# Kernel tuning notes

Hardware: AMD Instinct MI355X
Metric: run time of the kernel (lower is better)

The kernel has to match this reference:

```python
import jax, jax.numpy as jnp
import numpy as np

B, T, C = 2, 2048, 2048
NUM_HEADS, NUM_KV_HEADS, HEAD_DIM = 16, 4, 128
ROPE_THETA = 10000.0
SOFTCAP = 50.0


def sine_table(features, length, min_timescale=1.0, max_timescale=10000.0):
    fraction = jnp.arange(0, features, 2, dtype=jnp.float32) / features
    timescale = min_timescale * (max_timescale / min_timescale) ** fraction
    sinusoid = jnp.arange(length, dtype=jnp.float32)[:, None] / timescale[None, :]
    sinusoid = jnp.concatenate([sinusoid, sinusoid], axis=-1)
    return jnp.sin(sinusoid), jnp.cos(sinusoid)


def rotate_half(x):
    x1, x2 = jnp.split(x, 2, axis=-1)
    return jnp.concatenate([-x2, x1], axis=-1)


def setup_inputs() -> dict:
    key = jax.random.key(0)
    k1, k2, k3, k4, k5 = jax.random.split(key, 5)
    x = jax.random.normal(k1, (B, T, C), dtype=jnp.float32)
    mask = jnp.tril(jnp.ones((T, T), dtype=bool))[None, None]  # causal [1,1,T,T]
    mask = jnp.broadcast_to(mask, (B, 1, T, T))
    std = 0.02
    q_kernel = std * jax.random.normal(k2, (C, NUM_HEADS * HEAD_DIM), dtype=jnp.float32)
    k_kernel = std * jax.random.normal(k3, (C, NUM_KV_HEADS * HEAD_DIM), dtype=jnp.float32)
    v_kernel = std * jax.random.normal(k4, (C, NUM_KV_HEADS * HEAD_DIM), dtype=jnp.float32)
    out_kernel = std * jax.random.normal(k5, (NUM_HEADS * HEAD_DIM, C), dtype=jnp.float32)
    return {"x": x, "mask": mask, "q_kernel": q_kernel, "k_kernel": k_kernel,
            "v_kernel": v_kernel, "out_kernel": out_kernel}


def reference(x, mask, q_kernel, k_kernel, v_kernel, out_kernel):
    _, t, c = x.shape
    r = NUM_HEADS // NUM_KV_HEADS  # GQA group size
    qp = q_kernel.reshape(c, r, NUM_KV_HEADS, HEAD_DIM)
    kp = k_kernel.reshape(c, NUM_KV_HEADS, HEAD_DIM)
    vp = v_kernel.reshape(c, NUM_KV_HEADS, HEAD_DIM)
    op = out_kernel.reshape(r, NUM_KV_HEADS, HEAD_DIM, c)
    q = jnp.einsum('bsm,mrhk->brhsk', x, qp)   # [B,r,h,T,hd]
    k = jnp.einsum('bdm,mhk->bhdk', x, kp)     # [B,h,T,hd]
    v = jnp.einsum('bdm,mhv->bhdv', x, vp)     # [B,h,T,hd]
    sin, cos = sine_table(HEAD_DIM, t, max_timescale=ROPE_THETA)  # [T,hd]
    q = q * cos + rotate_half(q) * sin  # broadcast over leading dims (time at -2)
    k = k * cos + rotate_half(k) * sin
    scale = jax.lax.rsqrt(jnp.array(HEAD_DIM, dtype=x.dtype))
    qk = jnp.einsum('brhsk,bhdk->brhsd', q, k) * scale  # [B,r,h,T,T]
    qk = jnp.tanh(qk / SOFTCAP) * SOFTCAP  # logit softcap
    m = jnp.expand_dims(mask, axis=1)  # [B,1,1,T,T]
    qk = jax.nn.softmax(qk.astype(jnp.float32), where=m).astype(x.dtype)
    qkv = jnp.einsum('brhsd,bhdv->brhsv', qk, v)
    out = jnp.einsum('brhsv,rhvm->bsm', qkv, op)
    return out
```

## Files before the change

kernel.cpp:

```cpp
#include <hip/hip_runtime.h>
#include <hip/hip_bf16.h>

typedef __hip_bfloat16 bf16;
typedef __attribute__((ext_vector_type(8))) short bf16x8;
typedef __attribute__((ext_vector_type(4))) short bf16x4;
typedef __attribute__((ext_vector_type(4))) float f32x4;

#define BATCH 2
#define SEQ 2048
#define CDIM 2048
#define NH 16
#define NKV 4
#define HD 128
#define NQKV 3072

__device__ __forceinline__ float tof(float x)  { return x; }
__device__ __forceinline__ float tof(bf16 x)   { return __bfloat162float(x); }
__device__ __forceinline__ void  stf(float* p, float v) { *p = v; }
__device__ __forceinline__ void  stf(bf16* p,  float v) { *p = __float2bfloat16(v); }

__device__ __forceinline__ void gl_lds16(const bf16* g, bf16* l) {
    typedef const __attribute__((address_space(1))) unsigned int* gp_t;
    typedef __attribute__((address_space(3))) unsigned int* lp_t;
    __builtin_amdgcn_global_load_lds((gp_t)g, (lp_t)l, 16, 0, 0);
}

__device__ __forceinline__ f32x4 mfma16x16x16_bf16(bf16x4 a, bf16x4 b, f32x4 c) {
#if __has_builtin(__builtin_amdgcn_mfma_f32_16x16x16bf16_1k)
    return __builtin_amdgcn_mfma_f32_16x16x16bf16_1k(a, b, c, 0, 0, 0);
#else
    asm volatile("v_mfma_f32_16x16x16_bf16 %0, %1, %2, %0"
                 : "+v"(c) : "v"(a), "v"(b));
    return c;
#endif
}

__device__ __forceinline__ float fast_exp2(float x) {
#if __has_builtin(__builtin_amdgcn_exp2f)
    return __builtin_amdgcn_exp2f(x);
#else
    return exp2f(x);
#endif
}

__device__ __forceinline__ float softcap_exp(float u) {
    float t2 = u * u;
    float w = fmaf(t2, -1.328448e-7f, 0.12753101f);
    return fast_exp2(u * w);
}

__global__ __launch_bounds__(256) void f2b_kernel(const float* __restrict__ in,
                                                  bf16* __restrict__ out, int n4)
{
    int i = blockIdx.x * 256 + threadIdx.x;
    if (i >= n4) return;
    float4 v = *(const float4*)&in[(size_t)i * 4];
    bf16 o[4] = {__float2bfloat16(v.x), __float2bfloat16(v.y),
                 __float2bfloat16(v.z), __float2bfloat16(v.w)};
    *(ushort4*)&out[(size_t)i * 4] = *(ushort4*)o;
}

__global__ __launch_bounds__(256) void transpose_f2b_kernel(
    const float* __restrict__ in, bf16* __restrict__ out, int R, int Cn)
{
    __shared__ float tile[64][65];
    const int r0 = blockIdx.y * 64, c0 = blockIdx.x * 64;
    for (int f = threadIdx.x; f < 4096; f += 256) {
        int r = f >> 6, c = f & 63;
        tile[r][c] = in[(size_t)(r0 + r) * Cn + c0 + c];
    }
    __syncthreads();
    for (int f = threadIdx.x; f < 4096; f += 256) {
        int r = f >> 6, c = f & 63;
        out[(size_t)(c0 + r) * R + r0 + c] = __float2bfloat16(tile[c][r]);
    }
}

__global__ __launch_bounds__(256) void vtrans_kernel(
    const bf16* __restrict__ in, bf16* __restrict__ out)
{
    __shared__ bf16 tile[64][65];
    const int b = blockIdx.z;
    const int t0 = blockIdx.y * 64, c0 = blockIdx.x * 64;
    for (int f = threadIdx.x; f < 4096; f += 256) {
        int r = f >> 6, c = f & 63;
        tile[r][c] = in[(size_t)(b * SEQ + t0 + r) * (NKV * HD) + c0 + c];
    }
    __syncthreads();
    for (int f = threadIdx.x; f < 4096; f += 256) {
        int r = f >> 6, c = f & 63;
        out[(size_t)(b * NKV * HD + c0 + r) * SEQ + t0 + c] = tile[c][r];
    }
}

__global__ __launch_bounds__(256) void gemm_qkv_kernel(
    const bf16* __restrict__ A, const bf16* __restrict__ Bt,
    bf16* __restrict__ Qr, bf16* __restrict__ Kr, bf16* __restrict__ Vr,
    int M, int K)
{
    __shared__ __align__(16) bf16 As[128 * 32];
    __shared__ __align__(16) bf16 Bs[128 * 32];

    const int tid = threadIdx.x;
    const int lane = tid & 63;
    const int wave = tid >> 6;
    const int m0 = blockIdx.y * 128;
    const int n0 = blockIdx.x * 128;
    const int wm = (wave >> 1) * 64;
    const int wn = (wave & 1) * 64;
    const int quad = lane >> 4;
    const int l16 = lane & 15;

    const int srow = tid >> 2;
    const int scol = (tid & 3) * 8;
    const bf16* Ag0 = A  + (size_t)(m0 + srow) * K + scol;
    const bf16* Ag1 = A  + (size_t)(m0 + srow + 64) * K + scol;
    const bf16* Bg0 = Bt + (size_t)(n0 + srow) * K + scol;
    const bf16* Bg1 = Bt + (size_t)(n0 + srow + 64) * K + scol;

    f32x4 acc[4][4];
#pragma unroll
    for (int mi = 0; mi < 4; ++mi)
#pragma unroll
        for (int ni = 0; ni < 4; ++ni)
            acc[mi][ni] = (f32x4){0.f, 0.f, 0.f, 0.f};

    for (int kt = 0; kt < K; kt += 32) {
        __syncthreads();
        gl_lds16(Ag0 + kt, &As[tid * 8]);
        gl_lds16(Ag1 + kt, &As[2048 + tid * 8]);
        gl_lds16(Bg0 + kt, &Bs[tid * 8]);
        gl_lds16(Bg1 + kt, &Bs[2048 + tid * 8]);
        __syncthreads();

        bf16x8 a[4], b[4];
#pragma unroll
        for (int mi = 0; mi < 4; ++mi)
            a[mi] = *(const bf16x8*)&As[(wm + mi * 16 + l16) * 32 + quad * 8];
#pragma unroll
        for (int ni = 0; ni < 4; ++ni)
            b[ni] = *(const bf16x8*)&Bs[(wn + ni * 16 + l16) * 32 + quad * 8];
#pragma unroll
        for (int mi = 0; mi < 4; ++mi)
#pragma unroll
            for (int ni = 0; ni < 4; ++ni)
                acc[mi][ni] = __builtin_amdgcn_mfma_f32_16x16x32_bf16(
                    a[mi], b[ni], acc[mi][ni], 0, 0, 0);
    }

    bf16* Cp; int Nst, cbase;
    if (n0 < 2048)      { Cp = Qr; Nst = 2048; cbase = n0; }
    else if (n0 < 2560) { Cp = Kr; Nst = 512;  cbase = n0 - 2048; }
    else                { Cp = Vr; Nst = 512;  cbase = n0 - 2560; }

#pragma unroll
    for (int mi = 0; mi < 4; ++mi)
#pragma unroll
        for (int ni = 0; ni < 4; ++ni) {
            int col = cbase + wn + ni * 16 + l16;
#pragma unroll
            for (int r = 0; r < 4; ++r) {
                int row = m0 + wm + mi * 16 + quad * 4 + r;
                Cp[(size_t)row * Nst + col] = __float2bfloat16(acc[mi][ni][r]);
            }
        }
}

template <typename TC>
__global__ __launch_bounds__(256) void gemm_mfma_bt(
    const bf16* __restrict__ A, const bf16* __restrict__ Bt, TC* __restrict__ C,
    int M, int N, int K)
{
    __shared__ __align__(16) bf16 As[128 * 32];
    __shared__ __align__(16) bf16 Bs[128 * 32];

    const int tid = threadIdx.x;
    const int lane = tid & 63;
    const int wave = tid >> 6;
    const int m0 = blockIdx.y * 128;
    const int n0 = blockIdx.x * 128;
    const int wm = (wave >> 1) * 64;
    const int wn = (wave & 1) * 64;
    const int quad = lane >> 4;
    const int l16 = lane & 15;

    const int srow = tid >> 2;
    const int scol = (tid & 3) * 8;
    const bf16* Ag0 = A  + (size_t)(m0 + srow) * K + scol;
    const bf16* Ag1 = A  + (size_t)(m0 + srow + 64) * K + scol;
    const bf16* Bg0 = Bt + (size_t)(n0 + srow) * K + scol;
    const bf16* Bg1 = Bt + (size_t)(n0 + srow + 64) * K + scol;

    f32x4 acc[4][4];
#pragma unroll
    for (int mi = 0; mi < 4; ++mi)
#pragma unroll
        for (int ni = 0; ni < 4; ++ni)
            acc[mi][ni] = (f32x4){0.f, 0.f, 0.f, 0.f};

    for (int kt = 0; kt < K; kt += 32) {
        __syncthreads();
        gl_lds16(Ag0 + kt, &As[tid * 8]);
        gl_lds16(Ag1 + kt, &As[2048 + tid * 8]);
        gl_lds16(Bg0 + kt, &Bs[tid * 8]);
        gl_lds16(Bg1 + kt, &Bs[2048 + tid * 8]);
        __syncthreads();

        bf16x8 a[4], b[4];
#pragma unroll
        for (int mi = 0; mi < 4; ++mi)
            a[mi] = *(const bf16x8*)&As[(wm + mi * 16 + l16) * 32 + quad * 8];
#pragma unroll
        for (int ni = 0; ni < 4; ++ni)
            b[ni] = *(const bf16x8*)&Bs[(wn + ni * 16 + l16) * 32 + quad * 8];
#pragma unroll
        for (int mi = 0; mi < 4; ++mi)
#pragma unroll
            for (int ni = 0; ni < 4; ++ni)
                acc[mi][ni] = __builtin_amdgcn_mfma_f32_16x16x32_bf16(
                    a[mi], b[ni], acc[mi][ni], 0, 0, 0);
    }

#pragma unroll
    for (int mi = 0; mi < 4; ++mi)
#pragma unroll
        for (int ni = 0; ni < 4; ++ni) {
            int col = n0 + wn + ni * 16 + l16;
#pragma unroll
            for (int r = 0; r < 4; ++r) {
                int row = m0 + wm + mi * 16 + quad * 4 + r;
                stf(&C[(size_t)row * N + col], acc[mi][ni][r]);
            }
        }
}

__global__ __launch_bounds__(256) void rope_kernel(bf16* __restrict__ data,
                                                   int ncols, int total_pairs)
{
    int idx = blockIdx.x * 256 + threadIdx.x;
    if (idx >= total_pairs) return;
    int half = ncols >> 1;
    int row = idx / half;
    int p = idx - row * half;
    int head = p >> 6;
    int i = p & 63;
    int t = row & (SEQ - 1);
    float inv_ts = expf(-(float)i * 0.14391156831212787f);
    float angle = (float)t * inv_ts;
    float s, c;
    sincosf(angle, &s, &c);
    size_t base = (size_t)row * ncols + head * 128 + i;
    float x1 = __bfloat162float(data[base]);
    float x2 = __bfloat162float(data[base + 64]);
    data[base]      = __float2bfloat16(x1 * c - x2 * s);
    data[base + 64] = __float2bfloat16(x2 * c + x1 * s);
}

template <bool WA>
__device__ __forceinline__ void attn_tile_compute(
    const bf16* __restrict__ Ksr, const bf16* __restrict__ Vtsr,
    const bf16x8 (&qfA)[4], const bf16x8 (&qfB)[4],
    f32x4 (&OA)[8], f32x4 (&OB)[8], float& lsumA, float& lsumB,
    int quad, int l16, int ks, bool diagA, bool diagB, int qselA, int qselB)
{
    f32x4 sA[2], sB[2];
    bf16x4 pfA[2], pfB[2];
#pragma unroll
    for (int mt = 0; mt < 2; ++mt) {
        sB[mt] = (f32x4){0.f, 0.f, 0.f, 0.f};
        if constexpr (WA) sA[mt] = (f32x4){0.f, 0.f, 0.f, 0.f};
        const int krow = (ks * 32 + mt * 16 + l16) * 128;
#pragma unroll
        for (int kk = 0; kk < 4; ++kk) {
            bf16x8 kf = *(const bf16x8*)&Ksr[krow + (((kk * 4 + quad) ^ l16) * 8)];
            sB[mt] = __builtin_amdgcn_mfma_f32_16x16x32_bf16(
                kf, qfB[kk], sB[mt], 0, 0, 0);
            if constexpr (WA)
                sA[mt] = __builtin_amdgcn_mfma_f32_16x16x32_bf16(
                    kf, qfA[kk], sA[mt], 0, 0, 0);
        }
    }
#pragma unroll
    for (int mt = 0; mt < 2; ++mt) {
        bf16 pb[4];
#pragma unroll
        for (int r = 0; r < 4; ++r) {
            float p = softcap_exp(sB[mt][r]);
            if (diagB) {
                int kl = ks * 32 + mt * 16 + quad * 4 + r;
                p = (kl <= qselB) ? p : 0.f;
            }
            lsumB += p;
            pb[r] = __float2bfloat16(p);
        }
        pfB[mt] = *(bf16x4*)pb;
        if constexpr (WA) {
            bf16 pa[4];
#pragma unroll
            for (int r = 0; r < 4; ++r) {
                float p = softcap_exp(sA[mt][r]);
                if (diagA) {
                    int kl = ks * 32 + mt * 16 + quad * 4 + r;
                    p = (kl <= qselA) ? p : 0.f;
                }
                lsumA += p;
                pa[r] = __float2bfloat16(p);
            }
            pfA[mt] = *(bf16x4*)pa;
        }
    }
#pragma unroll
    for (int dj = 0; dj < 8; ++dj) {
        const int vrow = (dj * 16 + l16) * 64;
        const int dl7 = l16 & 7;
#pragma unroll
        for (int mt = 0; mt < 2; ++mt) {
            int c16 = ks * 4 + mt * 2 + (quad >> 1);
            bf16x4 vf = *(const bf16x4*)&Vtsr[vrow + ((c16 ^ dl7) << 3)
                                              + (quad & 1) * 4];
            OB[dj] = mfma16x16x16_bf16(vf, pfB[mt], OB[dj]);
            if constexpr (WA)
                OA[dj] = mfma16x16x16_bf16(vf, pfA[mt], OA[dj]);
        }
    }
}

__global__ __launch_bounds__(512, 2) void attn_mfma10_kernel(
    const bf16* __restrict__ Q, const bf16* __restrict__ K,
    const bf16* __restrict__ Vt, bf16* __restrict__ Att)
{
    __shared__ __align__(16) char smem[70144];

    const int tid = threadIdx.x;
    const int lane = tid & 63;
    const int w = tid >> 6;
    const int ks = w >> 2;
    const int hs = (w >> 1) & 1;
    const int qw = w & 1;
    const int quad = lane >> 4;
    const int l16 = lane & 15;
    const int bh = blockIdx.y;
    const int b   = bh >> 3;
    const int kvh = (bh >> 1) & 3;
    const int pr  = bh & 1;
    const int hq  = kvh + 4 * (pr * 2 + hs);
    const int qlo = blockIdx.x;
    const int qhi = 63 - qlo;
    const int ntlo = (qlo >> 1) + 1;
    const int nthi = (qhi >> 1) + 1;
    const int q0A = qlo * 32 + qw * 16;
    const int q0B = qhi * 32 + qw * 16;

    bf16x8 qfA[4], qfB[4];
    {
        size_t ra = (size_t)(b * SEQ + q0A + l16) * (NH * HD) + hq * HD;
        size_t rb = (size_t)(b * SEQ + q0B + l16) * (NH * HD) + hq * HD;
#pragma unroll
        for (int kk = 0; kk < 4; ++kk) {
            qfA[kk] = *(const bf16x8*)&Q[ra + kk * 32 + quad * 8];
            qfB[kk] = *(const bf16x8*)&Q[rb + kk * 32 + quad * 8];
        }
    }

    f32x4 OA[8], OB[8];
#pragma unroll
    for (int dj = 0; dj < 8; ++dj) {
        OA[dj] = (f32x4){0.f, 0.f, 0.f, 0.f};
        OB[dj] = (f32x4){0.f, 0.f, 0.f, 0.f};
    }
    float lsumA = 0.f, lsumB = 0.f;

    const int qselA = (qlo & 1) * 32 + qw * 16 + l16;
    const int qselB = (qhi & 1) * 32 + qw * 16 + l16;

    const int keyK = tid >> 4;
    const int chK  = (tid & 15) ^ (keyK & 15);
    const int dV   = tid >> 3;
    const int chV  = (tid & 7) ^ (dV & 7);
    const bf16* gK = K  + (size_t)(b * SEQ + keyK) * (NKV * HD) + kvh * HD + chK * 8;
    const bf16* gV = Vt + (size_t)((b * NKV + kvh) * HD + dV) * SEQ + chV * 8;

    {
        bf16* KsW  = (bf16*)smem;
        bf16* VtsW = (bf16*)(smem + 32768);
        gl_lds16(gK,                 KsW + tid * 8);
        gl_lds16(gK + 32 * NKV * HD, KsW + 4096 + tid * 8);
        gl_lds16(gV,                 VtsW + tid * 8);
        gl_lds16(gV + 64 * SEQ,      VtsW + 4096 + tid * 8);
    }
    __syncthreads();

    int cur = 0;
    for (int jt = 0; jt < nthi; ++jt) {
        if (jt + 1 < nthi) {
            gK += 64 * NKV * HD;
            gV += 64;
            bf16* KsW  = (bf16*)(smem + (cur ^ 1) * 16384);
            bf16* VtsW = (bf16*)(smem + 32768 + (cur ^ 1) * 16384);
            gl_lds16(gK,                 KsW + tid * 8);
            gl_lds16(gK + 32 * NKV * HD, KsW + 4096 + tid * 8);
            gl_lds16(gV,                 VtsW + tid * 8);
            gl_lds16(gV + 64 * SEQ,      VtsW + 4096 + tid * 8);
        }
        const bf16* Ksr  = (const bf16*)(smem + cur * 16384);
        const bf16* Vtsr = (const bf16*)(smem + 32768 + cur * 16384);
        const bool diagA = (jt == ntlo - 1);
        const bool diagB = (jt == nthi - 1);
        if (jt < ntlo)
            attn_tile_compute<true>(Ksr, Vtsr, qfA, qfB, OA, OB, lsumA, lsumB,
                                    quad, l16, ks, diagA, diagB, qselA, qselB);
        else
            attn_tile_compute<false>(Ksr, Vtsr, qfA, qfB, OA, OB, lsumA, lsumB,
                                     quad, l16, ks, diagA, diagB, qselA, qselB);
        __syncthreads();
        cur ^= 1;
    }

    float* Osh = (float*)smem;
    float* Lsh = (float*)(smem + 69632);
    const int p = hs * 2 + qw;
    const int ob = (p * 64 + lane) * 68;
    if (ks == 1) {
#pragma unroll
        for (int dj = 0; dj < 8; ++dj) {
            *(f32x4*)&Osh[ob + dj * 4]      = OA[dj];
            *(f32x4*)&Osh[ob + 32 + dj * 4] = OB[dj];
        }
        float vA = lsumA;
        vA += __shfl_xor(vA, 16);
        vA += __shfl_xor(vA, 32);
        float vB = lsumB;
        vB += __shfl_xor(vB, 16);
        vB += __shfl_xor(vB, 32);
        if (quad == 0) {
            Lsh[p * 32 + l16]      = vA;
            Lsh[p * 32 + 16 + l16] = vB;
        }
    }
    __syncthreads();
    if (ks == 0) {
        const int b2 = bh >> 3;
        {
            float v = lsumA;
            v += __shfl_xor(v, 16);
            v += __shfl_xor(v, 32);
            v += Lsh[p * 32 + l16];
            float inv = 1.f / v;
            size_t obase = (size_t)(b2 * SEQ + q0A + l16) * (NH * HD) + hq * HD;
#pragma unroll
            for (int dj = 0; dj < 8; ++dj) {
                f32x4 o = OA[dj] + *(const f32x4*)&Osh[ob + dj * 4];
                bf16 obuf[4];
#pragma unroll
                for (int r = 0; r < 4; ++r)
                    obuf[r] = __float2bfloat16(o[r] * inv);
                *(ushort4*)&Att[obase + dj * 16 + quad * 4] = *(ushort4*)obuf;
            }
        }
        {
            float v = lsumB;
            v += __shfl_xor(v, 16);
            v += __shfl_xor(v, 32);
            v += Lsh[p * 32 + 16 + l16];
            float inv = 1.f / v;
            size_t obase = (size_t)(b2 * SEQ + q0B + l16) * (NH * HD) + hq * HD;
#pragma unroll
            for (int dj = 0; dj < 8; ++dj) {
                f32x4 o = OB[dj] + *(const f32x4*)&Osh[ob + 32 + dj * 4];
                bf16 obuf[4];
#pragma unroll
                for (int r = 0; r < 4; ++r)
                    obuf[r] = __float2bfloat16(o[r] * inv);
                *(ushort4*)&Att[obase + dj * 16 + quad * 4] = *(ushort4*)obuf;
            }
        }
    }
}

extern "C" void kernel_launch(void* const* d_in, const int* in_sizes, int n_in,
                              void* d_out, int out_size, void* d_ws, size_t ws_size,
                              hipStream_t stream) {
    const float* x        = (const float*)d_in[0];
    const float* q_kernel = (const float*)d_in[2];
    const float* k_kernel = (const float*)d_in[3];
    const float* v_kernel = (const float*)d_in[4];
    const float* o_kernel = (const float*)d_in[5];
    float* out = (float*)d_out;

    const int M = BATCH * SEQ;
    char* ws = (char*)d_ws;
    bf16* xb   = (bf16*)ws;
    bf16* Att  = xb;
    bf16* wT   = (bf16*)(ws + 16777216);
    bf16* wTq  = wT;
    bf16* wTk  = wT + (size_t)2048 * 2048;
    bf16* wTv  = wT + (size_t)2560 * 2048;
    bf16* woT  = wT;
    bf16* Vt_g = (bf16*)(ws + 25165824);
    bf16* Qr   = (bf16*)(ws + 29360128);
    bf16* Kr   = (bf16*)(ws + 46137344);
    bf16* Vr   = (bf16*)(ws + 50331648);

    f2b_kernel<<<(M * CDIM / 4 + 255) / 256, 256, 0, stream>>>(x, xb, M * CDIM / 4);
    transpose_f2b_kernel<<<dim3((NH * HD) / 64, CDIM / 64), 256, 0, stream>>>(
        q_kernel, wTq, CDIM, NH * HD);
    transpose_f2b_kernel<<<dim3((NKV * HD) / 64, CDIM / 64), 256, 0, stream>>>(
        k_kernel, wTk, CDIM, NKV * HD);
    transpose_f2b_kernel<<<dim3((NKV * HD) / 64, CDIM / 64), 256, 0, stream>>>(
        v_kernel, wTv, CDIM, NKV * HD);

    gemm_qkv_kernel<<<dim3(NQKV / 128, M / 128), 256, 0, stream>>>(
        xb, wT, Qr, Kr, Vr, M, CDIM);

    transpose_f2b_kernel<<<dim3(CDIM / 64, CDIM / 64), 256, 0, stream>>>(
        o_kernel, woT, CDIM, CDIM);

    {
        int pairs_q = M * (NH * HD / 2);
        rope_kernel<<<pairs_q / 256, 256, 0, stream>>>(Qr, NH * HD, pairs_q);
        int pairs_k = M * (NKV * HD / 2);
        rope_kernel<<<pairs_k / 256, 256, 0, stream>>>(Kr, NKV * HD, pairs_k);
    }

    vtrans_kernel<<<dim3((NKV * HD) / 64, SEQ / 64, BATCH), 256, 0, stream>>>(Vr, Vt_g);

    attn_mfma10_kernel<<<dim3(SEQ / 64, BATCH * NKV * 2), 512, 0, stream>>>(
        Qr, Kr, Vt_g, Att);

    gemm_mfma_bt<float><<<dim3(CDIM / 128, M / 128), 256, 0, stream>>>(
        Att, woT, out, M, CDIM, CDIM);
}
```

Before: 384.5 us.

## Fuse Q RoPE into attention and write V transposed from QKV GEMM

Removes the standalone RoPE pass over Q by applying the rotation to Q fragments in registers at the start of the attention kernel, computing sin/cos on the fly. Removes the separate V transpose kernel by having the QKV GEMM epilogue store V directly in transposed [b,kvh,d,t] layout using 4-wide stores. This saves two launches and a full read/write of Q and of V. The cost is per-thread transcendental work (expf, sincosf) in the attention prologue, possible small numerical differences from the on-the-fly angle computation, and strided transposed stores from the GEMM.

```diff
diff --git a/kernel.cpp b/kernel.cpp
--- a/kernel.cpp
+++ b/kernel.cpp
@@ -49,6 +49,29 @@
     return fast_exp2(u * w);
 }
 
+__device__ __forceinline__ void rope_frags(bf16x8 (&qf)[4], float t, int quad) {
+#pragma unroll
+    for (int kk = 0; kk < 2; ++kk) {
+        union { bf16x8 v; short s[8]; } lo, hi;
+        lo.v = qf[kk]; hi.v = qf[kk + 2];
+#pragma unroll
+        for (int jj = 0; jj < 8; ++jj) {
+            int d = kk * 32 + quad * 8 + jj;
+            float inv_ts = expf(-(float)d * 0.14391156831212787f);
+            float ang = t * inv_ts;
+            float s, c;
+            sincosf(ang, &s, &c);
+            float x1 = __bfloat162float(*reinterpret_cast<bf16*>(&lo.s[jj]));
+            float x2 = __bfloat162float(*reinterpret_cast<bf16*>(&hi.s[jj]));
+            bf16 r1 = __float2bfloat16(x1 * c - x2 * s);
+            bf16 r2 = __float2bfloat16(x2 * c + x1 * s);
+            lo.s[jj] = *reinterpret_cast<short*>(&r1);
+            hi.s[jj] = *reinterpret_cast<short*>(&r2);
+        }
+        qf[kk] = lo.v; qf[kk + 2] = hi.v;
+    }
+}
+
 __global__ __launch_bounds__(256) void f2b_kernel(const float* __restrict__ in,
                                                   bf16* __restrict__ out, int n4)
 {
@@ -76,26 +99,9 @@
     }
 }
 
-__global__ __launch_bounds__(256) void vtrans_kernel(
-    const bf16* __restrict__ in, bf16* __restrict__ out)
-{
-    __shared__ bf16 tile[64][65];
-    const int b = blockIdx.z;
-    const int t0 = blockIdx.y * 64, c0 = blockIdx.x * 64;
-    for (int f = threadIdx.x; f < 4096; f += 256) {
-        int r = f >> 6, c = f & 63;
-        tile[r][c] = in[(size_t)(b * SEQ + t0 + r) * (NKV * HD) + c0 + c];
-    }
-    __syncthreads();
-    for (int f = threadIdx.x; f < 4096; f += 256) {
-        int r = f >> 6, c = f & 63;
-        out[(size_t)(b * NKV * HD + c0 + r) * SEQ + t0 + c] = tile[c][r];
-    }
-}
-
 __global__ __launch_bounds__(256) void gemm_qkv_kernel(
     const bf16* __restrict__ A, const bf16* __restrict__ Bt,
-    bf16* __restrict__ Qr, bf16* __restrict__ Kr, bf16* __restrict__ Vr,
+    bf16* __restrict__ Qr, bf16* __restrict__ Kr, bf16* __restrict__ Vt,
     int M, int K)
 {
     __shared__ __align__(16) bf16 As[128 * 32];
@@ -148,22 +154,39 @@
                     a[mi], b[ni], acc[mi][ni], 0, 0, 0);
     }
 
-    bf16* Cp; int Nst, cbase;
-    if (n0 < 2048)      { Cp = Qr; Nst = 2048; cbase = n0; }
-    else if (n0 < 2560) { Cp = Kr; Nst = 512;  cbase = n0 - 2048; }
-    else                { Cp = Vr; Nst = 512;  cbase = n0 - 2560; }
-
-#pragma unroll
-    for (int mi = 0; mi < 4; ++mi)
-#pragma unroll
-        for (int ni = 0; ni < 4; ++ni) {
-            int col = cbase + wn + ni * 16 + l16;
-#pragma unroll
-            for (int r = 0; r < 4; ++r) {
-                int row = m0 + wm + mi * 16 + quad * 4 + r;
-                Cp[(size_t)row * Nst + col] = __float2bfloat16(acc[mi][ni][r]);
-            }
-        }
+    if (n0 < 2560) {
+        bf16* Cp; int Nst, cbase;
+        if (n0 < 2048) { Cp = Qr; Nst = 2048; cbase = n0; }
+        else           { Cp = Kr; Nst = 512;  cbase = n0 - 2048; }
+#pragma unroll
+        for (int mi = 0; mi < 4; ++mi)
+#pragma unroll
+            for (int ni = 0; ni < 4; ++ni) {
+                int col = cbase + wn + ni * 16 + l16;
+#pragma unroll
+                for (int r = 0; r < 4; ++r) {
+                    int row = m0 + wm + mi * 16 + quad * 4 + r;
+                    Cp[(size_t)row * Nst + col] = __float2bfloat16(acc[mi][ni][r]);
+                }
+            }
+    } else {
+        const int cbase = n0 - 2560;
+#pragma unroll
+        for (int mi = 0; mi < 4; ++mi)
+#pragma unroll
+            for (int ni = 0; ni < 4; ++ni) {
+                int col = cbase + wn + ni * 16 + l16;
+                int kvh = col >> 7, d = col & 127;
+                int m = m0 + wm + mi * 16 + quad * 4;
+                int bb = m >> 11, t0 = m & 2047;
+                bf16 vb[4];
+#pragma unroll
+                for (int r = 0; r < 4; ++r)
+                    vb[r] = __float2bfloat16(acc[mi][ni][r]);
+                *(ushort4*)&Vt[((size_t)((bb * NKV + kvh) * HD + d)) * SEQ + t0] =
+                    *(ushort4*)vb;
+            }
+    }
 }
 
 template <typename TC>
@@ -325,7 +348,7 @@
     }
 }
 
-__global__ __launch_bounds__(512, 2) void attn_mfma10_kernel(
+__global__ __launch_bounds__(512, 2) void attn_mfma11_kernel(
     const bf16* __restrict__ Q, const bf16* __restrict__ K,
     const bf16* __restrict__ Vt, bf16* __restrict__ Att)
 {
@@ -360,6 +383,8 @@
             qfA[kk] = *(const bf16x8*)&Q[ra + kk * 32 + quad * 8];
             qfB[kk] = *(const bf16x8*)&Q[rb + kk * 32 + quad * 8];
         }
+        rope_frags(qfA, (float)(q0A + l16), quad);
+        rope_frags(qfB, (float)(q0B + l16), quad);
     }
 
     f32x4 OA[8], OB[8];
@@ -439,14 +464,13 @@
     }
     __syncthreads();
     if (ks == 0) {
-        const int b2 = bh >> 3;
         {
             float v = lsumA;
             v += __shfl_xor(v, 16);
             v += __shfl_xor(v, 32);
             v += Lsh[p * 32 + l16];
             float inv = 1.f / v;
-            size_t obase = (size_t)(b2 * SEQ + q0A + l16) * (NH * HD) + hq * HD;
+            size_t obase = (size_t)(b * SEQ + q0A + l16) * (NH * HD) + hq * HD;
 #pragma unroll
             for (int dj = 0; dj < 8; ++dj) {
                 f32x4 o = OA[dj] + *(const f32x4*)&Osh[ob + dj * 4];
@@ -463,7 +487,7 @@
             v += __shfl_xor(v, 32);
             v += Lsh[p * 32 + 16 + l16];
             float inv = 1.f / v;
-            size_t obase = (size_t)(b2 * SEQ + q0B + l16) * (NH * HD) + hq * HD;
+            size_t obase = (size_t)(b * SEQ + q0B + l16) * (NH * HD) + hq * HD;
 #pragma unroll
             for (int dj = 0; dj < 8; ++dj) {
                 f32x4 o = OB[dj] + *(const f32x4*)&Osh[ob + 32 + dj * 4];
@@ -496,10 +520,9 @@
     bf16* wTk  = wT + (size_t)2048 * 2048;
     bf16* wTv  = wT + (size_t)2560 * 2048;
     bf16* woT  = wT;
-    bf16* Vt_g = (bf16*)(ws + 25165824);
     bf16* Qr   = (bf16*)(ws + 29360128);
     bf16* Kr   = (bf16*)(ws + 46137344);
-    bf16* Vr   = (bf16*)(ws + 50331648);
+    bf16* Vt_g = (bf16*)(ws + 50331648);
 
     f2b_kernel<<<(M * CDIM / 4 + 255) / 256, 256, 0, stream>>>(x, xb, M * CDIM / 4);
     transpose_f2b_kernel<<<dim3((NH * HD) / 64, CDIM / 64), 256, 0, stream>>>(
@@ -510,21 +533,17 @@
         v_kernel, wTv, CDIM, NKV * HD);
 
     gemm_qkv_kernel<<<dim3(NQKV / 128, M / 128), 256, 0, stream>>>(
-        xb, wT, Qr, Kr, Vr, M, CDIM);
+        xb, wT, Qr, Kr, Vt_g, M, CDIM);
 
     transpose_f2b_kernel<<<dim3(CDIM / 64, CDIM / 64), 256, 0, stream>>>(
         o_kernel, woT, CDIM, CDIM);
 
     {
-        int pairs_q = M * (NH * HD / 2);
-        rope_kernel<<<pairs_q / 256, 256, 0, stream>>>(Qr, NH * HD, pairs_q);
         int pairs_k = M * (NKV * HD / 2);
         rope_kernel<<<pairs_k / 256, 256, 0, stream>>>(Kr, NKV * HD, pairs_k);
     }
 
-    vtrans_kernel<<<dim3((NKV * HD) / 64, SEQ / 64, BATCH), 256, 0, stream>>>(Vr, Vt_g);
-
-    attn_mfma10_kernel<<<dim3(SEQ / 64, BATCH * NKV * 2), 512, 0, stream>>>(
+    attn_mfma11_kernel<<<dim3(SEQ / 64, BATCH * NKV * 2), 512, 0, stream>>>(
         Qr, Kr, Vt_g, Att);
 
     gemm_mfma_bt<float><<<dim3(CDIM / 128, M / 128), 256, 0, stream>>>(
```

Result: faster. 371.5 us (-3.4%).
